# Kernel optimization log

Hardware: AMD Instinct MI355X
Metric: run time of the kernel (lower is better)

Reference implementation:

```python
import jax, jax.numpy as jnp
import numpy as np

N_NODES = 100_000
N_EDGES = 800_000
N_GRAPHS = 5_000
F_NODE = 11
F_EDGE = 4
H1 = 32   # conv1 out channels
H2 = 16   # conv2 out channels


def setup_inputs() -> dict:
    key = jax.random.key(0)
    ks = jax.random.split(key, 20)
    g = lambda i, shape, s=0.1: (jax.random.normal(ks[i], shape, dtype=jnp.float32) * s)
    inp = {
        "x": jax.random.normal(ks[0], (N_NODES, F_NODE), dtype=jnp.float32),
        "edge_index": jax.random.randint(ks[1], (2, N_EDGES), 0, N_NODES, dtype=jnp.int64),
        "edge_attr": jax.random.normal(ks[2], (N_EDGES, F_EDGE), dtype=jnp.float32),
        "batch": jnp.sort(jax.random.randint(ks[3], (N_NODES,), 0, N_GRAPHS, dtype=jnp.int64)),
        # conv1 edge MLP: 4 -> 32 -> 11*32
        "c1_w1": g(4, (F_EDGE, 32)), "c1_b1": jnp.zeros((32,), jnp.float32),
        "c1_w2": g(5, (32, F_NODE * H1)), "c1_b2": jnp.zeros((F_NODE * H1,), jnp.float32),
        "c1_root": g(6, (F_NODE, H1)), "c1_bias": jnp.zeros((H1,), jnp.float32),
        # conv2 edge MLP: 4 -> 32 -> 32*16
        "c2_w1": g(7, (F_EDGE, 32)), "c2_b1": jnp.zeros((32,), jnp.float32),
        "c2_w2": g(8, (32, H1 * H2)), "c2_b2": jnp.zeros((H1 * H2,), jnp.float32),
        "c2_root": g(9, (H1, H2)), "c2_bias": jnp.zeros((H2,), jnp.float32),
        # head
        "fc1_w": g(10, (H2, 32)), "fc1_b": jnp.zeros((32,), jnp.float32),
        "out_w": g(11, (32, 1)), "out_b": jnp.zeros((1,), jnp.float32),
    }
    return inp


def nnconv(x, src, dst, edge_attr, w1, b1, w2, b2, root, bias, c_in, c_out):
    # edge MLP -> per-edge weight matrix [E, c_in, c_out]
    h = jax.nn.relu(edge_attr @ w1 + b1)
    W = (h @ w2 + b2).reshape(-1, c_in, c_out)
    # gather source node features, per-edge matmul, scatter-add to targets
    msg = jnp.einsum("ei,eio->eo", x[src], W)
    agg = jax.ops.segment_sum(msg, dst, num_segments=x.shape[0])
    return agg + x @ root + bias


def reference(x, edge_index, edge_attr, batch,
              c1_w1, c1_b1, c1_w2, c1_b2, c1_root, c1_bias,
              c2_w1, c2_b1, c2_w2, c2_b2, c2_root, c2_bias,
              fc1_w, fc1_b, out_w, out_b):
    src, dst = edge_index[0], edge_index[1]
    h = jax.nn.relu(nnconv(x, src, dst, edge_attr, c1_w1, c1_b1, c1_w2, c1_b2,
                           c1_root, c1_bias, F_NODE, H1))
    h = jax.nn.relu(nnconv(h, src, dst, edge_attr, c2_w1, c2_b1, c2_w2, c2_b2,
                           c2_root, c2_bias, H1, H2))
    pooled = jax.ops.segment_sum(h, batch, num_segments=N_GRAPHS)  # global_add_pool
    h = jax.nn.relu(pooled @ fc1_w + fc1_b)
    return h @ out_w + out_b  # (B, 1)
```

## Files before the change

kernel.cpp:

```cpp
#include <hip/hip_runtime.h>
#include <hip/hip_fp16.h>

#define NNODES 100000
#define NEDGES 800000
#define NGRAPHS 5000
#define FN 11
#define FE 4
#define H1C 32
#define H2C 16

typedef _Float16 half8 __attribute__((ext_vector_type(8)));
typedef float f32x4 __attribute__((ext_vector_type(4)));

__device__ __forceinline__ void pk_atomic_add(_Float16* p, float a, float b) {
  __half2 v = __floats2half2_rn(a, b);
  unsafeAtomicAdd(reinterpret_cast<__half2*>(p), v);
}

__global__ __launch_bounds__(256) void k_init1(const float* __restrict__ x,
    const float* __restrict__ root, const float* __restrict__ bias,
    _Float16* __restrict__ agg1) {
  int t = blockIdx.x * 256 + threadIdx.x;
  int n = t >> 5, o = t & 31;
  if (n >= NNODES) return;
  float acc = bias[o];
  #pragma unroll
  for (int i = 0; i < FN; i++) acc += x[n * FN + i] * root[i * H1C + o];
  agg1[n * H1C + o] = (_Float16)acc;
}

__global__ __launch_bounds__(256) void k_prepB1(const float* __restrict__ w2,
    const float* __restrict__ b2, _Float16* __restrict__ B1h) {
  int t = blockIdx.x * 256 + threadIdx.x;
  if (t >= 2 * 12 * 64 * 8) return;
  int j = t & 7;
  int lane = (t >> 3) & 63;
  int rest = t >> 9;
  int step = rest % 12;
  int ot = rest / 12;
  int q = (lane >> 4) * 8 + j;
  int o = (lane & 15) + ot * 16;
  float v;
  if (step < 11) v = w2[q * (FN * H1C) + step * H1C + o];
  else v = (q < FN) ? b2[q * H1C + o] : 0.f;
  B1h[t] = (_Float16)v;
}

__global__ __launch_bounds__(256, 3) void k_edge1_mfma(
    const float* __restrict__ x, const int* __restrict__ ei,
    const float* __restrict__ ea, const float* __restrict__ w1,
    const float* __restrict__ b1, const _Float16* __restrict__ B1h,
    _Float16* __restrict__ agg1) {
  __shared__ _Float16 Bl[12288];
  __shared__ _Float16 h_sl[4][256][8];
  __shared__ _Float16 xs_sl[2][256][8];
  __shared__ int s_dst[256];
  int tid = threadIdx.x;
  {
    const int4* s = (const int4*)B1h;
    int4* d = (int4*)Bl;
    #pragma unroll
    for (int q = 0; q < 6; q++) d[q * 256 + tid] = s[q * 256 + tid];
  }
  int e = blockIdx.x * 256 + tid;
  int src = ei[e];
  s_dst[tid] = ei[NEDGES + e];
  float4 a4 = *reinterpret_cast<const float4*>(ea + e * 4);
  float h[32];
  #pragma unroll
  for (int k = 0; k < 32; k++) {
    float v = b1[k] + a4.x * w1[k] + a4.y * w1[32 + k] + a4.z * w1[64 + k] + a4.w * w1[96 + k];
    h[k] = v > 0.f ? v : 0.f;
  }
  #pragma unroll
  for (int s = 0; s < 4; s++) {
    half8 t8;
    #pragma unroll
    for (int j = 0; j < 8; j++) t8[j] = (_Float16)h[s * 8 + j];
    *reinterpret_cast<half8*>(&h_sl[s][tid][0]) = t8;
  }
  float xsv[FN];
  #pragma unroll
  for (int i = 0; i < FN; i++) xsv[i] = x[src * FN + i];
  #pragma unroll
  for (int s = 0; s < 2; s++) {
    half8 t8;
    #pragma unroll
    for (int j = 0; j < 8; j++) {
      int k = s * 8 + j;
      t8[j] = (k < FN) ? (_Float16)xsv[k] : (_Float16)0.f;
    }
    *reinterpret_cast<half8*>(&xs_sl[s][tid][0]) = t8;
  }
  __syncthreads();
  int lane = tid & 63;
  int w = tid >> 6;
  int halfk = lane >> 4;
  int er = lane & 15;
  #pragma unroll 1
  for (int g = 0; g < 4; g++) {
    int eb = w * 64 + g * 16;
    int el = eb + er;
    half8 hs8 = *reinterpret_cast<const half8*>(&h_sl[halfk][el][0]);
    half8 xs8;
    if (halfk < 2) xs8 = *reinterpret_cast<const half8*>(&xs_sl[halfk][el][0]);
    else xs8 = half8{};
    f32x4 acc0 = {0.f, 0.f, 0.f, 0.f};
    f32x4 acc1 = {0.f, 0.f, 0.f, 0.f};
    {
      half8 b0 = *reinterpret_cast<const half8*>(&Bl[11 * 512 + lane * 8]);
      half8 b1f = *reinterpret_cast<const half8*>(&Bl[6144 + 11 * 512 + lane * 8]);
      acc0 = __builtin_amdgcn_mfma_f32_16x16x32_f16(xs8, b0, acc0, 0, 0, 0);
      acc1 = __builtin_amdgcn_mfma_f32_16x16x32_f16(xs8, b1f, acc1, 0, 0, 0);
    }
    #pragma unroll
    for (int i = 0; i < FN; i++) {
      _Float16 xh = xs_sl[i >> 3][el][i & 7];
      half8 xsp;
      #pragma unroll
      for (int j = 0; j < 8; j++) xsp[j] = xh;
      half8 af = xsp * hs8;
      half8 b0 = *reinterpret_cast<const half8*>(&Bl[i * 512 + lane * 8]);
      half8 b1f = *reinterpret_cast<const half8*>(&Bl[6144 + i * 512 + lane * 8]);
      acc0 = __builtin_amdgcn_mfma_f32_16x16x32_f16(af, b0, acc0, 0, 0, 0);
      acc1 = __builtin_amdgcn_mfma_f32_16x16x32_f16(af, b1f, acc1, 0, 0, 0);
    }
    #pragma unroll
    for (int r = 0; r < 4; r++) {
      int d = s_dst[eb + halfk * 4 + r];
      float p0 = __shfl_xor(acc0[r], 1, 64);
      float p1 = __shfl_xor(acc1[r], 1, 64);
      int odd = er & 1;
      int ch = odd ? (16 + er - 1) : er;
      float lo = odd ? p1 : acc0[r];
      float hi = odd ? acc1[r] : p0;
      pk_atomic_add(&agg1[d * H1C + ch], lo, hi);
    }
  }
}

__global__ __launch_bounds__(256) void k_mid(const _Float16* __restrict__ agg1,
    const float* __restrict__ root2, const float* __restrict__ bias2,
    _Float16* __restrict__ h1h, _Float16* __restrict__ agg2) {
  int t = blockIdx.x * 256 + threadIdx.x;
  int n = t >> 4, o = t & 15;
  if (n >= NNODES) return;
  float hv[32];
  #pragma unroll
  for (int i = 0; i < 32; i++) {
    float v = (float)agg1[n * H1C + i];
    hv[i] = v > 0.f ? v : 0.f;
  }
  h1h[n * H1C + o] = (_Float16)hv[o];
  h1h[n * H1C + o + 16] = (_Float16)hv[o + 16];
  float acc = bias2[o];
  #pragma unroll
  for (int i = 0; i < 32; i++) acc += hv[i] * root2[i * H2C + o];
  agg2[n * H2C + o] = (_Float16)acc;
}

__global__ __launch_bounds__(256) void k_prepB2(const float* __restrict__ w2,
    _Float16* __restrict__ B2h) {
  int t = blockIdx.x * 256 + threadIdx.x;
  if (t >= 32 * 64 * 8) return;
  int kk = t >> 9;
  int l = (t >> 3) & 63;
  int j = t & 7;
  int i = (l >> 4) * 8 + j;
  int o = l & 15;
  B2h[t] = (_Float16)w2[(kk * 32 + i) * H2C + o];
}

__global__ __launch_bounds__(256, 3) void k_edge2_mfma(
    const _Float16* __restrict__ h1h, const int* __restrict__ ei,
    const float* __restrict__ ea, const float* __restrict__ w1,
    const float* __restrict__ b1, const _Float16* __restrict__ B2h,
    _Float16* __restrict__ agg2) {
  __shared__ _Float16 Bl[16384];
  __shared__ _Float16 h_lds[256][34];
  __shared__ int s_src[256];
  __shared__ int s_dst[256];
  int tid = threadIdx.x;
  {
    const int4* s = (const int4*)B2h;
    int4* d = (int4*)Bl;
    #pragma unroll
    for (int q = 0; q < 8; q++) d[q * 256 + tid] = s[q * 256 + tid];
  }
  int e = blockIdx.x * 256 + tid;
  s_src[tid] = ei[e];
  s_dst[tid] = ei[NEDGES + e];
  float4 a4 = *reinterpret_cast<const float4*>(ea + e * 4);
  #pragma unroll
  for (int k = 0; k < 32; k++) {
    float v = b1[k] + a4.x * w1[k] + a4.y * w1[32 + k] + a4.z * w1[64 + k] + a4.w * w1[96 + k];
    h_lds[tid][k] = (_Float16)(v > 0.f ? v : 0.f);
  }
  __syncthreads();
  int lane = tid & 63;
  int w = tid >> 6;
  int halfk = lane >> 4;
  int er = lane & 15;
  #pragma unroll 1
  for (int g = 0; g < 4; g++) {
    int eb = w * 64 + g * 16;
    int el = eb + er;
    int sn = s_src[el];
    half8 hsb = *reinterpret_cast<const half8*>(h1h + sn * H1C + halfk * 8);
    f32x4 acc = {0.f, 0.f, 0.f, 0.f};
    #pragma unroll
    for (int kk = 0; kk < 32; kk++) {
      _Float16 hv = h_lds[el][kk];
      half8 hsp;
      #pragma unroll
      for (int j = 0; j < 8; j++) hsp[j] = hv;
      half8 af = hsp * hsb;
      half8 bfrag = *reinterpret_cast<const half8*>(&Bl[(kk * 64 + lane) * 8]);
      acc = __builtin_amdgcn_mfma_f32_16x16x32_f16(af, bfrag, acc, 0, 0, 0);
    }
    #pragma unroll
    for (int r2 = 0; r2 < 4; r2 += 2) {
      int d_e = s_dst[eb + halfk * 4 + r2];
      int d_o = s_dst[eb + halfk * 4 + r2 + 1];
      float pe = __shfl_xor(acc[r2], 1, 64);
      float po = __shfl_xor(acc[r2 + 1], 1, 64);
      int odd = er & 1;
      int d = odd ? d_o : d_e;
      int ch = odd ? (er - 1) : er;
      float lo = odd ? po : acc[r2];
      float hi = odd ? acc[r2 + 1] : pe;
      pk_atomic_add(&agg2[d * H2C + ch], lo, hi);
    }
  }
}

__global__ __launch_bounds__(256) void k_pool(const _Float16* __restrict__ agg2,
    const int* __restrict__ batch, float* __restrict__ pooled) {
  int t = blockIdx.x * 256 + threadIdx.x;
  int n = t >> 4, o = t & 15;
  if (n >= NNODES) return;
  float v = (float)agg2[n * H2C + o];
  v = v > 0.f ? v : 0.f;
  atomicAdd(&pooled[batch[n] * H2C + o], v);
}

__global__ __launch_bounds__(256) void k_head(const float* __restrict__ pooled,
    const float* __restrict__ fc1w, const float* __restrict__ fc1b,
    const float* __restrict__ outw, const float* __restrict__ outb,
    float* __restrict__ out) {
  int g = blockIdx.x * 256 + threadIdx.x;
  if (g >= NGRAPHS) return;
  float p[H2C];
  #pragma unroll
  for (int i = 0; i < H2C; i++) p[i] = pooled[g * H2C + i];
  float acc = outb[0];
  #pragma unroll
  for (int o = 0; o < H1C; o++) {
    float v = fc1b[o];
    #pragma unroll
    for (int i = 0; i < H2C; i++) v += p[i] * fc1w[i * H1C + o];
    v = v > 0.f ? v : 0.f;
    acc += v * outw[o];
  }
  out[g] = acc;
}

extern "C" void kernel_launch(void* const* d_in, const int* in_sizes, int n_in,
                              void* d_out, int out_size, void* d_ws, size_t ws_size,
                              hipStream_t stream) {
  const float* x      = (const float*)d_in[0];
  const int*   ei     = (const int*)d_in[1];
  const float* ea     = (const float*)d_in[2];
  const int*   batch  = (const int*)d_in[3];
  const float* c1w1   = (const float*)d_in[4];
  const float* c1b1   = (const float*)d_in[5];
  const float* c1w2   = (const float*)d_in[6];
  const float* c1b2   = (const float*)d_in[7];
  const float* c1root = (const float*)d_in[8];
  const float* c1bias = (const float*)d_in[9];
  const float* c2w1   = (const float*)d_in[10];
  const float* c2b1   = (const float*)d_in[11];
  const float* c2w2   = (const float*)d_in[12];
  const float* c2b2   = (const float*)d_in[13];
  const float* c2root = (const float*)d_in[14];
  const float* c2bias = (const float*)d_in[15];
  const float* fc1w   = (const float*)d_in[16];
  const float* fc1b   = (const float*)d_in[17];
  const float* outw   = (const float*)d_in[18];
  const float* outb   = (const float*)d_in[19];
  float* out = (float*)d_out;

  _Float16*  agg1   = (_Float16*)d_ws;
  _Float16*  h1h    = agg1 + NNODES * H1C;
  _Float16*  agg2   = h1h + NNODES * H1C;
  float*     pooled = (float*)(agg2 + NNODES * H2C);
  _Float16*  B2h    = (_Float16*)(pooled + NGRAPHS * H2C);
  _Float16*  B1h    = B2h + 32 * 64 * 8;

  hipMemsetAsync(pooled, 0, NGRAPHS * H2C * sizeof(float), stream);

  k_init1<<<(NNODES * H1C + 255) / 256, 256, 0, stream>>>(x, c1root, c1bias, agg1);
  k_prepB1<<<48, 256, 0, stream>>>(c1w2, c1b2, B1h);
  k_prepB2<<<64, 256, 0, stream>>>(c2w2, B2h);
  k_edge1_mfma<<<NEDGES / 256, 256, 0, stream>>>(x, ei, ea, c1w1, c1b1, B1h, agg1);
  k_mid<<<(NNODES * H2C + 255) / 256, 256, 0, stream>>>(agg1, c2root, c2bias, h1h, agg2);
  k_edge2_mfma<<<NEDGES / 256, 256, 0, stream>>>(h1h, ei, ea, c2w1, c2b1, B2h, agg2);
  k_pool<<<(NNODES * H2C + 255) / 256, 256, 0, stream>>>(agg2, batch, pooled);
  k_head<<<(NGRAPHS + 255) / 256, 256, 0, stream>>>(pooled, fc1w, fc1b, outw, outb, out);
}
```

Baseline: 158.6 us.

## Interleave four edge groups per wave in MFMA loops and merge prep kernels

Both edge kernels now process their four 16-edge groups at once. Each B fragment is loaded from LDS once per k-step and reused across four independent MFMA accumulator chains, and the global gathers in edge2 are issued up front. This is meant to hide MFMA dependency latency and cut redundant LDS reads, at the cost of more live registers, which could hurt the 3-blocks-per-CU occupancy target. The two weight-prep kernels are also merged into one launch to save a kernel launch.

```diff
diff --git a/kernel.cpp b/kernel.cpp
--- a/kernel.cpp
+++ b/kernel.cpp
@@ -29,21 +29,32 @@
   agg1[n * H1C + o] = (_Float16)acc;
 }
 
-__global__ __launch_bounds__(256) void k_prepB1(const float* __restrict__ w2,
-    const float* __restrict__ b2, _Float16* __restrict__ B1h) {
+__global__ __launch_bounds__(256) void k_prep(const float* __restrict__ c1w2,
+    const float* __restrict__ c1b2, _Float16* __restrict__ B1h,
+    const float* __restrict__ c2w2, _Float16* __restrict__ B2h) {
   int t = blockIdx.x * 256 + threadIdx.x;
-  if (t >= 2 * 12 * 64 * 8) return;
-  int j = t & 7;
-  int lane = (t >> 3) & 63;
-  int rest = t >> 9;
-  int step = rest % 12;
-  int ot = rest / 12;
-  int q = (lane >> 4) * 8 + j;
-  int o = (lane & 15) + ot * 16;
-  float v;
-  if (step < 11) v = w2[q * (FN * H1C) + step * H1C + o];
-  else v = (q < FN) ? b2[q * H1C + o] : 0.f;
-  B1h[t] = (_Float16)v;
+  if (t < 2 * 12 * 64 * 8) {
+    int j = t & 7;
+    int lane = (t >> 3) & 63;
+    int rest = t >> 9;
+    int step = rest % 12;
+    int ot = rest / 12;
+    int q = (lane >> 4) * 8 + j;
+    int o = (lane & 15) + ot * 16;
+    float v;
+    if (step < 11) v = c1w2[q * (FN * H1C) + step * H1C + o];
+    else v = (q < FN) ? c1b2[q * H1C + o] : 0.f;
+    B1h[t] = (_Float16)v;
+  } else {
+    int t2 = t - 2 * 12 * 64 * 8;
+    if (t2 >= 32 * 64 * 8) return;
+    int kk = t2 >> 9;
+    int l = (t2 >> 3) & 63;
+    int j = t2 & 7;
+    int i = (l >> 4) * 8 + j;
+    int o = l & 15;
+    B2h[t2] = (_Float16)c2w2[(kk * 32 + i) * H2C + o];
+  }
 }
 
 __global__ __launch_bounds__(256, 3) void k_edge1_mfma(
@@ -97,43 +108,54 @@
   int w = tid >> 6;
   int halfk = lane >> 4;
   int er = lane & 15;
-  #pragma unroll 1
+  half8 hs8[4], xs8v[4];
+  f32x4 acc0[4], acc1[4];
+  #pragma unroll
   for (int g = 0; g < 4; g++) {
-    int eb = w * 64 + g * 16;
-    int el = eb + er;
-    half8 hs8 = *reinterpret_cast<const half8*>(&h_sl[halfk][el][0]);
-    half8 xs8;
-    if (halfk < 2) xs8 = *reinterpret_cast<const half8*>(&xs_sl[halfk][el][0]);
-    else xs8 = half8{};
-    f32x4 acc0 = {0.f, 0.f, 0.f, 0.f};
-    f32x4 acc1 = {0.f, 0.f, 0.f, 0.f};
-    {
-      half8 b0 = *reinterpret_cast<const half8*>(&Bl[11 * 512 + lane * 8]);
-      half8 b1f = *reinterpret_cast<const half8*>(&Bl[6144 + 11 * 512 + lane * 8]);
-      acc0 = __builtin_amdgcn_mfma_f32_16x16x32_f16(xs8, b0, acc0, 0, 0, 0);
-      acc1 = __builtin_amdgcn_mfma_f32_16x16x32_f16(xs8, b1f, acc1, 0, 0, 0);
-    }
-    #pragma unroll
-    for (int i = 0; i < FN; i++) {
+    int el = w * 64 + g * 16 + er;
+    hs8[g] = *reinterpret_cast<const half8*>(&h_sl[halfk][el][0]);
+    if (halfk < 2) xs8v[g] = *reinterpret_cast<const half8*>(&xs_sl[halfk][el][0]);
+    else xs8v[g] = half8{};
+    acc0[g] = f32x4{0.f, 0.f, 0.f, 0.f};
+    acc1[g] = f32x4{0.f, 0.f, 0.f, 0.f};
+  }
+  {
+    half8 b0 = *reinterpret_cast<const half8*>(&Bl[11 * 512 + lane * 8]);
+    half8 b1f = *reinterpret_cast<const half8*>(&Bl[6144 + 11 * 512 + lane * 8]);
+    #pragma unroll
+    for (int g = 0; g < 4; g++) {
+      acc0[g] = __builtin_amdgcn_mfma_f32_16x16x32_f16(xs8v[g], b0, acc0[g], 0, 0, 0);
+      acc1[g] = __builtin_amdgcn_mfma_f32_16x16x32_f16(xs8v[g], b1f, acc1[g], 0, 0, 0);
+    }
+  }
+  #pragma unroll
+  for (int i = 0; i < FN; i++) {
+    half8 b0 = *reinterpret_cast<const half8*>(&Bl[i * 512 + lane * 8]);
+    half8 b1f = *reinterpret_cast<const half8*>(&Bl[6144 + i * 512 + lane * 8]);
+    #pragma unroll
+    for (int g = 0; g < 4; g++) {
+      int el = w * 64 + g * 16 + er;
       _Float16 xh = xs_sl[i >> 3][el][i & 7];
       half8 xsp;
       #pragma unroll
       for (int j = 0; j < 8; j++) xsp[j] = xh;
-      half8 af = xsp * hs8;
-      half8 b0 = *reinterpret_cast<const half8*>(&Bl[i * 512 + lane * 8]);
-      half8 b1f = *reinterpret_cast<const half8*>(&Bl[6144 + i * 512 + lane * 8]);
-      acc0 = __builtin_amdgcn_mfma_f32_16x16x32_f16(af, b0, acc0, 0, 0, 0);
-      acc1 = __builtin_amdgcn_mfma_f32_16x16x32_f16(af, b1f, acc1, 0, 0, 0);
-    }
+      half8 af = xsp * hs8[g];
+      acc0[g] = __builtin_amdgcn_mfma_f32_16x16x32_f16(af, b0, acc0[g], 0, 0, 0);
+      acc1[g] = __builtin_amdgcn_mfma_f32_16x16x32_f16(af, b1f, acc1[g], 0, 0, 0);
+    }
+  }
+  #pragma unroll
+  for (int g = 0; g < 4; g++) {
+    int eb = w * 64 + g * 16;
     #pragma unroll
     for (int r = 0; r < 4; r++) {
       int d = s_dst[eb + halfk * 4 + r];
-      float p0 = __shfl_xor(acc0[r], 1, 64);
-      float p1 = __shfl_xor(acc1[r], 1, 64);
+      float p0 = __shfl_xor(acc0[g][r], 1, 64);
+      float p1 = __shfl_xor(acc1[g][r], 1, 64);
       int odd = er & 1;
       int ch = odd ? (16 + er - 1) : er;
-      float lo = odd ? p1 : acc0[r];
-      float hi = odd ? acc1[r] : p0;
+      float lo = odd ? p1 : acc0[g][r];
+      float hi = odd ? acc1[g][r] : p0;
       pk_atomic_add(&agg1[d * H1C + ch], lo, hi);
     }
   }
@@ -157,18 +179,6 @@
   #pragma unroll
   for (int i = 0; i < 32; i++) acc += hv[i] * root2[i * H2C + o];
   agg2[n * H2C + o] = (_Float16)acc;
-}
-
-__global__ __launch_bounds__(256) void k_prepB2(const float* __restrict__ w2,
-    _Float16* __restrict__ B2h) {
-  int t = blockIdx.x * 256 + threadIdx.x;
-  if (t >= 32 * 64 * 8) return;
-  int kk = t >> 9;
-  int l = (t >> 3) & 63;
-  int j = t & 7;
-  int i = (l >> 4) * 8 + j;
-  int o = l & 15;
-  B2h[t] = (_Float16)w2[(kk * 32 + i) * H2C + o];
 }
 
 __global__ __launch_bounds__(256, 3) void k_edge2_mfma(
@@ -201,34 +211,43 @@
   int w = tid >> 6;
   int halfk = lane >> 4;
   int er = lane & 15;
-  #pragma unroll 1
+  half8 hsb[4];
+  f32x4 acc[4];
+  #pragma unroll
   for (int g = 0; g < 4; g++) {
-    int eb = w * 64 + g * 16;
-    int el = eb + er;
+    int el = w * 64 + g * 16 + er;
     int sn = s_src[el];
-    half8 hsb = *reinterpret_cast<const half8*>(h1h + sn * H1C + halfk * 8);
-    f32x4 acc = {0.f, 0.f, 0.f, 0.f};
-    #pragma unroll
-    for (int kk = 0; kk < 32; kk++) {
+    hsb[g] = *reinterpret_cast<const half8*>(h1h + sn * H1C + halfk * 8);
+    acc[g] = f32x4{0.f, 0.f, 0.f, 0.f};
+  }
+  #pragma unroll 8
+  for (int kk = 0; kk < 32; kk++) {
+    half8 bfrag = *reinterpret_cast<const half8*>(&Bl[(kk * 64 + lane) * 8]);
+    #pragma unroll
+    for (int g = 0; g < 4; g++) {
+      int el = w * 64 + g * 16 + er;
       _Float16 hv = h_lds[el][kk];
       half8 hsp;
       #pragma unroll
       for (int j = 0; j < 8; j++) hsp[j] = hv;
-      half8 af = hsp * hsb;
-      half8 bfrag = *reinterpret_cast<const half8*>(&Bl[(kk * 64 + lane) * 8]);
-      acc = __builtin_amdgcn_mfma_f32_16x16x32_f16(af, bfrag, acc, 0, 0, 0);
-    }
+      half8 af = hsp * hsb[g];
+      acc[g] = __builtin_amdgcn_mfma_f32_16x16x32_f16(af, bfrag, acc[g], 0, 0, 0);
+    }
+  }
+  #pragma unroll
+  for (int g = 0; g < 4; g++) {
+    int eb = w * 64 + g * 16;
     #pragma unroll
     for (int r2 = 0; r2 < 4; r2 += 2) {
       int d_e = s_dst[eb + halfk * 4 + r2];
       int d_o = s_dst[eb + halfk * 4 + r2 + 1];
-      float pe = __shfl_xor(acc[r2], 1, 64);
-      float po = __shfl_xor(acc[r2 + 1], 1, 64);
+      float pe = __shfl_xor(acc[g][r2], 1, 64);
+      float po = __shfl_xor(acc[g][r2 + 1], 1, 64);
       int odd = er & 1;
       int d = odd ? d_o : d_e;
       int ch = odd ? (er - 1) : er;
-      float lo = odd ? po : acc[r2];
-      float hi = odd ? acc[r2 + 1] : pe;
+      float lo = odd ? po : acc[g][r2];
+      float hi = odd ? acc[g][r2 + 1] : pe;
       pk_atomic_add(&agg2[d * H2C + ch], lo, hi);
     }
   }
@@ -300,8 +319,7 @@
   hipMemsetAsync(pooled, 0, NGRAPHS * H2C * sizeof(float), stream);
 
   k_init1<<<(NNODES * H1C + 255) / 256, 256, 0, stream>>>(x, c1root, c1bias, agg1);
-  k_prepB1<<<48, 256, 0, stream>>>(c1w2, c1b2, B1h);
-  k_prepB2<<<64, 256, 0, stream>>>(c2w2, B2h);
+  k_prep<<<112, 256, 0, stream>>>(c1w2, c1b2, B1h, c2w2, B2h);
   k_edge1_mfma<<<NEDGES / 256, 256, 0, stream>>>(x, ei, ea, c1w1, c1b1, B1h, agg1);
   k_mid<<<(NNODES * H2C + 255) / 256, 256, 0, stream>>>(agg1, c2root, c2bias, h1h, agg2);
   k_edge2_mfma<<<NEDGES / 256, 256, 0, stream>>>(h1h, ei, ea, c2w1, c2b1, B2h, agg2);
```

Result: slower. 163.3 us (+2.9%).

## Fold root transform into mid kernel, merge prep kernels, vectorize edge2 LDS hidden

Applied to the files above, without the earlier changes.

Removes the k_init1 pass that wrote x@root1+bias into agg1, zeroing agg1 with a memset and computing the root term inside k_mid through a shared-memory tile. The two weight-prep kernels are merged into one launch. In edge2, the per-edge hidden features are stored as half8 vectors and read into registers once per group instead of as 32 scalar LDS reads. Together these cut kernel launches and one global pass over agg1, at the cost of extra x reads in k_mid.

```diff
diff --git a/kernel.cpp b/kernel.cpp
--- a/kernel.cpp
+++ b/kernel.cpp
@@ -17,33 +17,32 @@
   unsafeAtomicAdd(reinterpret_cast<__half2*>(p), v);
 }
 
-__global__ __launch_bounds__(256) void k_init1(const float* __restrict__ x,
-    const float* __restrict__ root, const float* __restrict__ bias,
-    _Float16* __restrict__ agg1) {
+__global__ __launch_bounds__(256) void k_prep(const float* __restrict__ c1w2,
+    const float* __restrict__ c1b2, _Float16* __restrict__ B1h,
+    const float* __restrict__ c2w2, _Float16* __restrict__ B2h) {
   int t = blockIdx.x * 256 + threadIdx.x;
-  int n = t >> 5, o = t & 31;
-  if (n >= NNODES) return;
-  float acc = bias[o];
-  #pragma unroll
-  for (int i = 0; i < FN; i++) acc += x[n * FN + i] * root[i * H1C + o];
-  agg1[n * H1C + o] = (_Float16)acc;
-}
-
-__global__ __launch_bounds__(256) void k_prepB1(const float* __restrict__ w2,
-    const float* __restrict__ b2, _Float16* __restrict__ B1h) {
-  int t = blockIdx.x * 256 + threadIdx.x;
-  if (t >= 2 * 12 * 64 * 8) return;
-  int j = t & 7;
-  int lane = (t >> 3) & 63;
-  int rest = t >> 9;
-  int step = rest % 12;
-  int ot = rest / 12;
-  int q = (lane >> 4) * 8 + j;
-  int o = (lane & 15) + ot * 16;
-  float v;
-  if (step < 11) v = w2[q * (FN * H1C) + step * H1C + o];
-  else v = (q < FN) ? b2[q * H1C + o] : 0.f;
-  B1h[t] = (_Float16)v;
+  if (t < 2 * 12 * 64 * 8) {
+    int j = t & 7;
+    int lane = (t >> 3) & 63;
+    int rest = t >> 9;
+    int step = rest % 12;
+    int ot = rest / 12;
+    int q = (lane >> 4) * 8 + j;
+    int o = (lane & 15) + ot * 16;
+    float v;
+    if (step < 11) v = c1w2[q * (FN * H1C) + step * H1C + o];
+    else v = (q < FN) ? c1b2[q * H1C + o] : 0.f;
+    B1h[t] = (_Float16)v;
+  } else {
+    int t2 = t - 2 * 12 * 64 * 8;
+    if (t2 >= 32 * 64 * 8) return;
+    int kk = t2 >> 9;
+    int l = (t2 >> 3) & 63;
+    int j = t2 & 7;
+    int i = (l >> 4) * 8 + j;
+    int o = l & 15;
+    B2h[t2] = (_Float16)c2w2[(kk * 32 + i) * H2C + o];
+  }
 }
 
 __global__ __launch_bounds__(256, 3) void k_edge1_mfma(
@@ -139,16 +138,32 @@
   }
 }
 
-__global__ __launch_bounds__(256) void k_mid(const _Float16* __restrict__ agg1,
-    const float* __restrict__ root2, const float* __restrict__ bias2,
-    _Float16* __restrict__ h1h, _Float16* __restrict__ agg2) {
-  int t = blockIdx.x * 256 + threadIdx.x;
+__global__ __launch_bounds__(256) void k_mid(const float* __restrict__ x,
+    const _Float16* __restrict__ agg1, const float* __restrict__ root1,
+    const float* __restrict__ bias1, const float* __restrict__ root2,
+    const float* __restrict__ bias2, _Float16* __restrict__ h1h,
+    _Float16* __restrict__ agg2) {
+  __shared__ float sbase[16][33];
+  int tid = threadIdx.x;
+  int t = blockIdx.x * 256 + tid;
   int n = t >> 4, o = t & 15;
-  if (n >= NNODES) return;
+  int nl = tid >> 4;
+  {
+    float b0 = bias1[o], b16 = bias1[o + 16];
+    #pragma unroll
+    for (int i = 0; i < FN; i++) {
+      float xv = x[n * FN + i];
+      b0 += xv * root1[i * H1C + o];
+      b16 += xv * root1[i * H1C + o + 16];
+    }
+    sbase[nl][o] = b0;
+    sbase[nl][o + 16] = b16;
+  }
+  __syncthreads();
   float hv[32];
   #pragma unroll
   for (int i = 0; i < 32; i++) {
-    float v = (float)agg1[n * H1C + i];
+    float v = (float)agg1[n * H1C + i] + sbase[nl][i];
     hv[i] = v > 0.f ? v : 0.f;
   }
   h1h[n * H1C + o] = (_Float16)hv[o];
@@ -157,18 +172,6 @@
   #pragma unroll
   for (int i = 0; i < 32; i++) acc += hv[i] * root2[i * H2C + o];
   agg2[n * H2C + o] = (_Float16)acc;
-}
-
-__global__ __launch_bounds__(256) void k_prepB2(const float* __restrict__ w2,
-    _Float16* __restrict__ B2h) {
-  int t = blockIdx.x * 256 + threadIdx.x;
-  if (t >= 32 * 64 * 8) return;
-  int kk = t >> 9;
-  int l = (t >> 3) & 63;
-  int j = t & 7;
-  int i = (l >> 4) * 8 + j;
-  int o = l & 15;
-  B2h[t] = (_Float16)w2[(kk * 32 + i) * H2C + o];
 }
 
 __global__ __launch_bounds__(256, 3) void k_edge2_mfma(
@@ -177,7 +180,7 @@
     const float* __restrict__ b1, const _Float16* __restrict__ B2h,
     _Float16* __restrict__ agg2) {
   __shared__ _Float16 Bl[16384];
-  __shared__ _Float16 h_lds[256][34];
+  __shared__ _Float16 h_sl2[4][256][8];
   __shared__ int s_src[256];
   __shared__ int s_dst[256];
   int tid = threadIdx.x;
@@ -192,9 +195,15 @@
   s_dst[tid] = ei[NEDGES + e];
   float4 a4 = *reinterpret_cast<const float4*>(ea + e * 4);
   #pragma unroll
-  for (int k = 0; k < 32; k++) {
-    float v = b1[k] + a4.x * w1[k] + a4.y * w1[32 + k] + a4.z * w1[64 + k] + a4.w * w1[96 + k];
-    h_lds[tid][k] = (_Float16)(v > 0.f ? v : 0.f);
+  for (int s = 0; s < 4; s++) {
+    half8 t8;
+    #pragma unroll
+    for (int j = 0; j < 8; j++) {
+      int k = s * 8 + j;
+      float v = b1[k] + a4.x * w1[k] + a4.y * w1[32 + k] + a4.z * w1[64 + k] + a4.w * w1[96 + k];
+      t8[j] = (_Float16)(v > 0.f ? v : 0.f);
+    }
+    *reinterpret_cast<half8*>(&h_sl2[s][tid][0]) = t8;
   }
   __syncthreads();
   int lane = tid & 63;
@@ -207,10 +216,17 @@
     int el = eb + er;
     int sn = s_src[el];
     half8 hsb = *reinterpret_cast<const half8*>(h1h + sn * H1C + halfk * 8);
+    half8 hr0 = *reinterpret_cast<const half8*>(&h_sl2[0][el][0]);
+    half8 hr1 = *reinterpret_cast<const half8*>(&h_sl2[1][el][0]);
+    half8 hr2 = *reinterpret_cast<const half8*>(&h_sl2[2][el][0]);
+    half8 hr3 = *reinterpret_cast<const half8*>(&h_sl2[3][el][0]);
     f32x4 acc = {0.f, 0.f, 0.f, 0.f};
     #pragma unroll
     for (int kk = 0; kk < 32; kk++) {
-      _Float16 hv = h_lds[el][kk];
+      _Float16 hv = (kk < 8) ? hr0[kk & 7]
+                  : (kk < 16) ? hr1[kk & 7]
+                  : (kk < 24) ? hr2[kk & 7]
+                  : hr3[kk & 7];
       half8 hsp;
       #pragma unroll
       for (int j = 0; j < 8; j++) hsp[j] = hv;
@@ -298,13 +314,13 @@
   _Float16*  B1h    = B2h + 32 * 64 * 8;
 
   hipMemsetAsync(pooled, 0, NGRAPHS * H2C * sizeof(float), stream);
-
-  k_init1<<<(NNODES * H1C + 255) / 256, 256, 0, stream>>>(x, c1root, c1bias, agg1);
-  k_prepB1<<<48, 256, 0, stream>>>(c1w2, c1b2, B1h);
-  k_prepB2<<<64, 256, 0, stream>>>(c2w2, B2h);
+  hipMemsetAsync(agg1, 0, (size_t)NNODES * H1C * sizeof(_Float16), stream);
+
+  k_prep<<<112, 256, 0, stream>>>(c1w2, c1b2, B1h, c2w2, B2h);
   k_edge1_mfma<<<NEDGES / 256, 256, 0, stream>>>(x, ei, ea, c1w1, c1b1, B1h, agg1);
-  k_mid<<<(NNODES * H2C + 255) / 256, 256, 0, stream>>>(agg1, c2root, c2bias, h1h, agg2);
+  k_mid<<<NNODES * H2C / 256, 256, 0, stream>>>(x, agg1, c1root, c1bias,
+                                                c2root, c2bias, h1h, agg2);
   k_edge2_mfma<<<NEDGES / 256, 256, 0, stream>>>(h1h, ei, ea, c2w1, c2b1, B2h, agg2);
-  k_pool<<<(NNODES * H2C + 255) / 256, 256, 0, stream>>>(agg2, batch, pooled);
+  k_pool<<<NNODES * H2C / 256, 256, 0, stream>>>(agg2, batch, pooled);
   k_head<<<(NGRAPHS + 255) / 256, 256, 0, stream>>>(pooled, fc1w, fc1b, outw, outb, out);
 }
```

New measurement: 156.5 us. No clear change (-1.3%).
